# Kernel tuning notes

Measured on AMD Instinct MI355X. Metric: run time of the kernel, lower is better.

The kernel has to match this reference:

```python
import jax, jax.numpy as jnp
import numpy as np

B, E, DIM = 8, 2048, 512
KERNEL = 8
DECAY_CONSTANT = 1.0


def _forward(x, weight, bias, decay_value):
    # x: (B, E, S) with S == dim; weight: (K, S); bias: (S,); decay_value: (2, 1)
    K, dim = weight.shape
    Bb, Ee, S = x.shape
    i = jnp.arange(dim)[:, None]
    j = jnp.arange(dim)[None, :]
    # decayed upper-triangular weight: W[k, i, j] = weight[k, j] * dv^((j-i)/c) for j >= i
    dv = jnp.clip(decay_value[1, 0], 0.9, 1.0)
    d = dv ** ((j - i).astype(x.dtype) / DECAY_CONSTANT)  # (S, S)
    W = jnp.where(j >= i, weight[:, None, :] * d[None], jnp.zeros((), x.dtype))  # (K, S, S)
    p = K - 1
    padded = jnp.pad(x, ((0, 0), (p, p), (0, 0)))  # zero-pad sequence axis
    # shifted stack: stacked[b, k, e] = x[b, e + k - (K-1)] (zeros out of range) -> causal taps
    stacked = jnp.stack([padded[:, k:Ee + k] for k in range(K)], axis=1)  # (B, K, E, S)
    out = jnp.einsum('bkei,kij->bej', stacked, W) + bias
    return out


def setup_inputs() -> dict:
    key = jax.random.key(0)
    k1, k2 = jax.random.split(key)
    x = jax.random.normal(k1, (B, E, DIM), dtype=jnp.float32)
    weight = jax.random.normal(k2, (KERNEL, DIM), dtype=jnp.float32)
    bias = jnp.zeros((DIM,), dtype=jnp.float32)
    decay_value = jnp.ones((2, 1), dtype=jnp.float32)
    return {"x": x, "weight": weight, "bias": bias, "decay_value": decay_value}


def reference(x, weight, bias, decay_value):
    return _forward(x, weight, bias, decay_value)
```

## Files before the change

### kernel.cpp

```cpp
#include <hip/hip_runtime.h>


#define B_    8
#define E_    2048
#define DIM_  512
#define K_    8
#define SE_   8
#define NR_   (SE_ + K_ - 1)

__global__ __launch_bounds__(256) void krl_win(
    const float* __restrict__ x,
    const float* __restrict__ weight,
    const float* __restrict__ bias,
    const float* __restrict__ decay,
    float* __restrict__ out)
{
    const int t    = threadIdx.x;
    const int lane = t & 63;
    const int wave = t >> 6;
    const int wid  = blockIdx.x * 4 + wave;
    const int b    = wid >> 8;
    const int e0   = (wid & 255) << 3;

    float dv = decay[1];
    dv = fminf(fmaxf(dv, 0.9f), 1.0f);
    const float dv2 = dv * dv;
    const float dv4 = dv2 * dv2;
    const float dv8 = dv4 * dv4;

    const int jf = lane * 8;

    float wv[K_][8];
    #pragma unroll
    for (int k = 0; k < K_; ++k) {
        const float4 p0 = *(const float4*)(weight + k * DIM_ + jf);
        const float4 p1 = *(const float4*)(weight + k * DIM_ + jf + 4);
        wv[k][0] = p0.x; wv[k][1] = p0.y; wv[k][2] = p0.z; wv[k][3] = p0.w;
        wv[k][4] = p1.x; wv[k][5] = p1.y; wv[k][6] = p1.z; wv[k][7] = p1.w;
    }
    const float4 bi0 = *(const float4*)(bias + jf);
    const float4 bi1 = *(const float4*)(bias + jf + 4);

    float a[SE_][8];
    #pragma unroll
    for (int m = 0; m < SE_; ++m)
        #pragma unroll
        for (int j = 0; j < 8; ++j) a[m][j] = 0.f;

    const float* xb = x + (size_t)b * E_ * DIM_ + jf;
    float*       ob = out + ((size_t)b * E_ + e0) * DIM_ + jf;

    #pragma unroll
    for (int r = 0; r < NR_; ++r) {
        const int eg = e0 - (K_ - 1) + r;
        if (eg >= 0) {
            const float4* xp = (const float4*)(xb + (size_t)eg * DIM_);
            const float4 a0 = xp[0];
            const float4 a1 = xp[1];
            const float xv[8] = {a0.x, a0.y, a0.z, a0.w, a1.x, a1.y, a1.z, a1.w};

            float tl[8];
            tl[0] = xv[0];
            #pragma unroll
            for (int m = 1; m < 8; ++m) tl[m] = fmaf(dv, tl[m - 1], xv[m]);

            float v  = tl[7];
            float ap = dv8;
            #pragma unroll
            for (int off = 1; off < 64; off <<= 1) {
                float up = __shfl_up(v, off, 64);
                if (lane >= off) v = fmaf(ap, up, v);
                ap *= ap;
            }
            float carry = __shfl_up(v, 1, 64);
            if (lane == 0) carry = 0.f;
            float dp = dv;
            #pragma unroll
            for (int m = 0; m < 8; ++m) { tl[m] = fmaf(dp, carry, tl[m]); dp *= dv; }

            const int mlo = (r - (K_ - 1)) < 0 ? 0 : (r - (K_ - 1));
            const int mhi = r < (SE_ - 1) ? r : (SE_ - 1);
            #pragma unroll
            for (int m = 0; m < SE_; ++m) {
                if (m >= mlo && m <= mhi) {
                    const int k = r - m;
                    #pragma unroll
                    for (int j = 0; j < 8; ++j)
                        a[m][j] = fmaf(wv[k][j], tl[j], a[m][j]);
                }
            }
        }
        if (r >= K_ - 1) {
            const int m = r - (K_ - 1);
            float4 o0 = make_float4(a[m][0] + bi0.x, a[m][1] + bi0.y,
                                    a[m][2] + bi0.z, a[m][3] + bi0.w);
            float4 o1 = make_float4(a[m][4] + bi1.x, a[m][5] + bi1.y,
                                    a[m][6] + bi1.z, a[m][7] + bi1.w);
            *(float4*)(ob + (size_t)m * DIM_)     = o0;
            *(float4*)(ob + (size_t)m * DIM_ + 4) = o1;
        }
    }
}

extern "C" void kernel_launch(void* const* d_in, const int* in_sizes, int n_in,
                              void* d_out, int out_size, void* d_ws, size_t ws_size,
                              hipStream_t stream) {
    const float* x      = (const float*)d_in[0];
    const float* weight = (const float*)d_in[1];
    const float* bias   = (const float*)d_in[2];
    const float* decay  = (const float*)d_in[3];
    float* out = (float*)d_out;

    krl_win<<<dim3((B_ * (E_ / SE_)) / 4), dim3(256), 0, stream>>>(
        x, weight, bias, decay, out);
}
```

Before: 91.82 us.

## Stage weights and bias in LDS and halve rows per wave

Weights and bias now load cooperatively into shared memory per block, replacing the 64 per-thread weight registers, and launch bounds request 4 blocks per CU. The outputs per wave drop from 8 to 4, doubling the grid. Fewer registers should raise occupancy and hide memory latency. The cost is more redundant work, since each wave now recomputes 11 scanned rows to produce 4 outputs instead of 15 for 8, plus LDS reads in the inner loop and a block barrier.

New measurement: 95.69 us. 1.04x slower.

```diff
diff --git a/kernel.cpp b/kernel.cpp
--- a/kernel.cpp
+++ b/kernel.cpp
@@ -5,22 +5,34 @@
 #define E_    2048
 #define DIM_  512
 #define K_    8
-#define SE_   8
+#define SE_   4
 #define NR_   (SE_ + K_ - 1)
 
-__global__ __launch_bounds__(256) void krl_win(
+__global__ __launch_bounds__(256, 4) void krl_win(
     const float* __restrict__ x,
     const float* __restrict__ weight,
     const float* __restrict__ bias,
     const float* __restrict__ decay,
     float* __restrict__ out)
 {
+    __shared__ float wlds[K_][DIM_];
+    __shared__ float blds[DIM_];
+
     const int t    = threadIdx.x;
     const int lane = t & 63;
     const int wave = t >> 6;
+
+    {
+        const float4* wsrc = (const float4*)weight;
+        float4*       wdst = (float4*)&wlds[0][0];
+        #pragma unroll
+        for (int i = 0; i < 4; ++i) wdst[t + 256 * i] = wsrc[t + 256 * i];
+        if (t < 128) ((float4*)blds)[t] = ((const float4*)bias)[t];
+    }
+
     const int wid  = blockIdx.x * 4 + wave;
-    const int b    = wid >> 8;
-    const int e0   = (wid & 255) << 3;
+    const int b    = wid >> 9;
+    const int e0   = (wid & 511) << 2;
 
     float dv = decay[1];
     dv = fminf(fmaxf(dv, 0.9f), 1.0f);
@@ -30,17 +42,6 @@
 
     const int jf = lane * 8;
 
-    float wv[K_][8];
-    #pragma unroll
-    for (int k = 0; k < K_; ++k) {
-        const float4 p0 = *(const float4*)(weight + k * DIM_ + jf);
-        const float4 p1 = *(const float4*)(weight + k * DIM_ + jf + 4);
-        wv[k][0] = p0.x; wv[k][1] = p0.y; wv[k][2] = p0.z; wv[k][3] = p0.w;
-        wv[k][4] = p1.x; wv[k][5] = p1.y; wv[k][6] = p1.z; wv[k][7] = p1.w;
-    }
-    const float4 bi0 = *(const float4*)(bias + jf);
-    const float4 bi1 = *(const float4*)(bias + jf + 4);
-
     float a[SE_][8];
     #pragma unroll
     for (int m = 0; m < SE_; ++m)
@@ -49,6 +50,8 @@
 
     const float* xb = x + (size_t)b * E_ * DIM_ + jf;
     float*       ob = out + ((size_t)b * E_ + e0) * DIM_ + jf;
+
+    __syncthreads();
 
     #pragma unroll
     for (int r = 0; r < NR_; ++r) {
@@ -78,24 +81,31 @@
             #pragma unroll
             for (int m = 0; m < 8; ++m) { tl[m] = fmaf(dp, carry, tl[m]); dp *= dv; }
 
-            const int mlo = (r - (K_ - 1)) < 0 ? 0 : (r - (K_ - 1));
-            const int mhi = r < (SE_ - 1) ? r : (SE_ - 1);
             #pragma unroll
             for (int m = 0; m < SE_; ++m) {
-                if (m >= mlo && m <= mhi) {
+                if (m <= r && r - m <= K_ - 1) {
                     const int k = r - m;
-                    #pragma unroll
-                    for (int j = 0; j < 8; ++j)
-                        a[m][j] = fmaf(wv[k][j], tl[j], a[m][j]);
+                    const float4 w0 = *(const float4*)(&wlds[k][jf]);
+                    const float4 w1 = *(const float4*)(&wlds[k][jf + 4]);
+                    a[m][0] = fmaf(w0.x, tl[0], a[m][0]);
+                    a[m][1] = fmaf(w0.y, tl[1], a[m][1]);
+                    a[m][2] = fmaf(w0.z, tl[2], a[m][2]);
+                    a[m][3] = fmaf(w0.w, tl[3], a[m][3]);
+                    a[m][4] = fmaf(w1.x, tl[4], a[m][4]);
+                    a[m][5] = fmaf(w1.y, tl[5], a[m][5]);
+                    a[m][6] = fmaf(w1.z, tl[6], a[m][6]);
+                    a[m][7] = fmaf(w1.w, tl[7], a[m][7]);
                 }
             }
         }
         if (r >= K_ - 1) {
             const int m = r - (K_ - 1);
-            float4 o0 = make_float4(a[m][0] + bi0.x, a[m][1] + bi0.y,
-                                    a[m][2] + bi0.z, a[m][3] + bi0.w);
-            float4 o1 = make_float4(a[m][4] + bi1.x, a[m][5] + bi1.y,
-                                    a[m][6] + bi1.z, a[m][7] + bi1.w);
+            const float4 b0 = *(const float4*)(&blds[jf]);
+            const float4 b1 = *(const float4*)(&blds[jf + 4]);
+            float4 o0 = make_float4(a[m][0] + b0.x, a[m][1] + b0.y,
+                                    a[m][2] + b0.z, a[m][3] + b0.w);
+            float4 o1 = make_float4(a[m][4] + b1.x, a[m][5] + b1.y,
+                                    a[m][6] + b1.z, a[m][7] + b1.w);
             *(float4*)(ob + (size_t)m * DIM_)     = o0;
             *(float4*)(ob + (size_t)m * DIM_ + 4) = o1;
         }
```
